# Kernel optimization log

Measured on AMD Instinct MI355X. Metric: run time of the kernel, lower is better.

## Reference

```python
import math
import jax, jax.numpy as jnp
import numpy as np

B, T = 65536, 34
VOCAB, TOK_DIM, POS_DIM, D_MODEL, FFN_DIM, HEAD_DIM = 14, 2, 3, 5, 2, 5
EPS = 1e-5

def _pos_flat_idx():
    # replicate _build_pos_map: 10 digits, Z_HI, 10 digits, Z_HI, 10 digits, special0, special1
    sources, indices = [], []
    for _ in range(3):
        for i in range(10):
            sources.append(0); indices.append(i)
        sources.append(2); indices.append(len([s for s in sources if s == 2]) - 1)
    # fix: the torch code appends (2,0),(2,1) after first two digit blocks and (1,0),(2,2) after the third
    sources, indices = [], []
    for i in range(10): sources.append(0); indices.append(i)
    sources.append(2); indices.append(0)
    for i in range(10): sources.append(0); indices.append(i)
    sources.append(2); indices.append(1)
    for i in range(10): sources.append(0); indices.append(i)
    sources.append(1); indices.append(0)
    sources.append(2); indices.append(2)
    src = np.array(sources); idx = np.array(indices)
    # table layout: rows 0..9 digit_pos, row 10 z_hi_pos, rows 11..13 special (learned0, learned1, eos)
    offs = np.array([0, 10, 11])
    return offs[src] + idx  # (34,)

POS_FLAT = jnp.asarray(_pos_flat_idx())
CAUSAL = jnp.tril(jnp.ones((T, T), dtype=bool))

def _rms(x, w):
    return x * jax.lax.rsqrt(jnp.mean(x * x, -1, keepdims=True) + EPS) * w

def setup_inputs():
    key = jax.random.key(0)
    ks = jax.random.split(key, 16)
    n = lambda i, shape: jax.random.normal(ks[i], shape, jnp.float32) * 0.5
    return {
        'idx': jax.random.randint(ks[0], (B, T), 0, VOCAB),
        'tok_emb': n(1, (VOCAB, TOK_DIM)),
        'spiral_amp': jnp.float32(1.0),
        'spiral_phase': jnp.float32(0.1),
        'spiral_slope': jnp.float32(1.0 / 9.0),
        'spiral_offset': jnp.float32(0.05),
        'pos_corr_slope': jnp.float32(0.01),
        'pos_corr_intercept': jnp.float32(0.02),
        'z_hi_pos': n(2, (1, POS_DIM)),
        'special_pos': n(3, (2, POS_DIM)),
        'q_w': n(4, (HEAD_DIM, POS_DIM)),
        'v_w': n(5, (HEAD_DIM, TOK_DIM)),
        'out_A': n(6, (HEAD_DIM, 2)),
        'out_B': n(7, (2, D_MODEL)),
        'q_phase': n(8, (1,)),
        'ln1_w': jnp.ones((D_MODEL,), jnp.float32),
        'ln2_w': jnp.ones((D_MODEL,), jnp.float32),
        'lnf_w': jnp.ones((D_MODEL,), jnp.float32),
        'fc1_w': n(9, (FFN_DIM, D_MODEL)),
        'fc1_b': n(10, (FFN_DIM,)),
        'fc2_w': n(11, (D_MODEL, FFN_DIM)),
        'fc2_b': n(12, (D_MODEL,)),
        'head_w': n(13, (TOK_DIM, D_MODEL)),
    }

def reference(idx, tok_emb, spiral_amp, spiral_phase, spiral_slope, spiral_offset,
              pos_corr_slope, pos_corr_intercept, z_hi_pos, special_pos,
              q_w, v_w, out_A, out_B, q_phase, ln1_w, ln2_w, lnf_w,
              fc1_w, fc1_b, fc2_w, fc2_b, head_w):
    # learned spiral digit positions (10, 3)
    i = jnp.arange(10, dtype=jnp.float32)
    angle = 2.0 * math.pi * i / 10.0 + spiral_phase
    base = jnp.stack([spiral_amp * jnp.cos(angle),
                      spiral_amp * jnp.sin(angle),
                      spiral_slope * i + spiral_offset], -1)
    corr = pos_corr_intercept + pos_corr_slope * i
    digit_pos = base * (1.0 + corr)[:, None]
    table = jnp.concatenate([digit_pos, z_hi_pos, special_pos,
                             jnp.zeros((1, POS_DIM), jnp.float32)], 0)  # (14, 3)
    pos = table[POS_FLAT]  # (T, 3)

    tok = tok_emb[idx]  # (B, T, 2)
    x = jnp.concatenate([tok, jnp.broadcast_to(pos, (idx.shape[0], T, POS_DIM))], -1)  # (B,T,5)

    h = _rms(x, ln1_w)
    q = jnp.einsum('btp,dp->btd', h[..., TOK_DIM:], q_w)  # (B,T,5)
    k = q  # q_proj applied to same input for both q and k
    v = jnp.einsum('btp,dp->btd', h[..., :TOK_DIM], v_w)  # (B,T,5)

    # per-head 2D rotation on first 4 dims (HEAD_DIM//2 = 2 pairs), dim 4 unchanged
    c, s = jnp.cos(q_phase[0]), jnp.sin(q_phase[0])
    q0, q1 = q[..., 0:4:2], q[..., 1:4:2]
    q_rot = jnp.concatenate([
        jnp.stack([q0 * c - q1 * s, q0 * s + q1 * c], -1).reshape(q.shape[:-1] + (4,)),
        q[..., 4:]], -1)

    att = jnp.einsum('btd,bsd->bts', q_rot, k) / math.sqrt(HEAD_DIM)
    att = jnp.where(CAUSAL, att, -jnp.inf)
    att = jax.nn.softmax(att, -1)
    out = jnp.einsum('bts,bsd->btd', att, v)  # (B,T,5)

    x = x + (out @ out_A) @ out_B  # low-rank out_proj
    hh = _rms(x, ln2_w)
    x = x + (jax.nn.gelu(hh @ fc1_w.T + fc1_b, approximate=False) @ fc2_w.T + fc2_b)
    x = _rms(x, lnf_w)
    return (x @ head_w.T) @ tok_emb.T  # (B, T, 14)
```

## Files before the change

kernel.cpp:

```cpp
#include <hip/hip_runtime.h>
#include <math.h>

#define T_SEQ 34
#define NTOK 14
#define NE (T_SEQ * NTOK)
#define ROWS 32
#define BLK 512
#define RP1 (ROWS + 1)

__global__ __launch_bounds__(BLK) void micro_fused_kernel(
    const int* __restrict__ idx,
    const float* __restrict__ tok_emb,
    const float* __restrict__ s_amp, const float* __restrict__ s_phase,
    const float* __restrict__ s_slope, const float* __restrict__ s_offset,
    const float* __restrict__ pc_slope, const float* __restrict__ pc_int,
    const float* __restrict__ z_hi, const float* __restrict__ spec,
    const float* __restrict__ q_w, const float* __restrict__ v_w,
    const float* __restrict__ out_A, const float* __restrict__ out_B,
    const float* __restrict__ q_phase,
    const float* __restrict__ ln1_w, const float* __restrict__ ln2_w,
    const float* __restrict__ lnf_w,
    const float* __restrict__ fc1_w, const float* __restrict__ fc1_b,
    const float* __restrict__ fc2_w, const float* __restrict__ fc2_b,
    const float* __restrict__ head_w,
    float* __restrict__ out, int N)
{
    __shared__ float4 H4[NE];
    __shared__ float  H1f[NE];
    __shared__ float4 C3[NE];
    __shared__ float4 Gm[T_SEQ * ROWS];
    __shared__ float  G1[T_SEQ * ROWS];
    __shared__ float2 Av[T_SEQ * RP1];
    __shared__ int    toks[ROWS * T_SEQ];
    __shared__ float PosT[T_SEQ * 3];
    __shared__ float TE[NTOK * 2];
    __shared__ float PMs[10];
    __shared__ float Ws[5 * NTOK];
    __shared__ float ln2s[5], lnfs[5], fc1ws[10], fc1bs[2], fc2ws[10], fc2bs[5];

    const int tid = threadIdx.x;
    const int b0 = blockIdx.x * ROWS;
    const int elemBase = b0 * T_SEQ;

    for (int i = tid; i < ROWS * T_SEQ; i += BLK) {
        int g = elemBase + i;
        toks[i] = (g < N) ? idx[g] : 0;
    }

    if (tid < NE) {
        const float amp = s_amp[0], ph = s_phase[0], slp = s_slope[0], off = s_offset[0];
        const float pcs = pc_slope[0], pci = pc_int[0];
        const float cph = cosf(q_phase[0]), sph = sinf(q_phase[0]);
        const float cscale = 0.44721359549995793f * 1.4426950408889634f;
        const int e = tid;
        const int t = e / NTOK, tk = e - t * NTOK;
        float px, py, pz;
        if (t == 33)      { px = 0.f;     py = 0.f;     pz = 0.f; }
        else if (t == 32) { px = z_hi[0]; py = z_hi[1]; pz = z_hi[2]; }
        else if (t == 10) { px = spec[0]; py = spec[1]; pz = spec[2]; }
        else if (t == 21) { px = spec[3]; py = spec[4]; pz = spec[5]; }
        else {
            int i = (t < 10) ? t : (t < 21 ? t - 11 : t - 22);
            float fi = (float)i;
            float ang = 0.62831853071795864769f * fi + ph;
            float mlt = 1.f + pci + pcs * fi;
            px = amp * cosf(ang) * mlt;
            py = amp * sinf(ang) * mlt;
            pz = (slp * fi + off) * mlt;
        }
        if (tk == 0) { PosT[t*3] = px; PosT[t*3+1] = py; PosT[t*3+2] = pz; }
        float x0 = tok_emb[tk * 2], x1 = tok_emb[tk * 2 + 1];
        float ssum = x0*x0 + x1*x1 + px*px + py*py + pz*pz;
        float rn = rsqrtf(ssum * 0.2f + 1e-5f);
        float h0 = x0 * rn * ln1_w[0], h1 = x1 * rn * ln1_w[1];
        float h2 = px * rn * ln1_w[2], h3 = py * rn * ln1_w[3], h4 = pz * rn * ln1_w[4];
        float q0 = q_w[0]  * h2 + q_w[1]  * h3 + q_w[2]  * h4;
        float q1 = q_w[3]  * h2 + q_w[4]  * h3 + q_w[5]  * h4;
        float q2 = q_w[6]  * h2 + q_w[7]  * h3 + q_w[8]  * h4;
        float q3 = q_w[9]  * h2 + q_w[10] * h3 + q_w[11] * h4;
        float q4 = q_w[12] * h2 + q_w[13] * h3 + q_w[14] * h4;
        float r0 = q0 * cph - q1 * sph, r1 = q0 * sph + q1 * cph;
        float r2c = q2 * cph - q3 * sph, r3 = q2 * sph + q3 * cph;
        float c0 = (r0*q_w[0] + r1*q_w[3] + r2c*q_w[6] + r3*q_w[9]  + q4*q_w[12]) * cscale;
        float c1 = (r0*q_w[1] + r1*q_w[4] + r2c*q_w[7] + r3*q_w[10] + q4*q_w[13]) * cscale;
        float c2 = (r0*q_w[2] + r1*q_w[5] + r2c*q_w[8] + r3*q_w[11] + q4*q_w[14]) * cscale;
        H4[e] = make_float4(h2, h3, h4, h0);
        H1f[e] = h1;
        C3[e] = make_float4(c0, c1, c2, 0.f);
    }
    if (tid < 28) TE[tid] = tok_emb[tid];
    if (tid < 70) {
        int d = tid / NTOK, v = tid - d * NTOK;
        Ws[tid] = head_w[d] * tok_emb[v * 2] + head_w[5 + d] * tok_emb[v * 2 + 1];
    }
    if (tid < 10) {
        int j = tid >> 1, c = tid & 1;
        float acc = 0.f;
        for (int i = 0; i < 5; ++i) {
            float m5 = out_A[i*2] * out_B[j] + out_A[i*2+1] * out_B[5 + j];
            acc += m5 * v_w[i*2 + c];
        }
        PMs[tid] = acc;
    }
    if (tid < 5)  { ln2s[tid] = ln2_w[tid]; lnfs[tid] = lnf_w[tid]; fc2bs[tid] = fc2_b[tid]; }
    if (tid < 10) { fc1ws[tid] = fc1_w[tid]; fc2ws[tid] = fc2_w[tid]; }
    if (tid < 2)  { fc1bs[tid] = fc1_b[tid]; }

    __syncthreads();

    for (int i = tid; i < T_SEQ * ROWS; i += BLK) {
        int s = i >> 5;
        int r = i & (ROWS - 1);
        int tok = toks[r * T_SEQ + s];
        int e = s * NTOK + tok;
        Gm[i] = H4[e];
        G1[i] = H1f[e];
    }
    __syncthreads();

    for (int ii = tid; ii < T_SEQ * ROWS; ii += BLK) {
        int t = ii >> 5;
        int r = ii & (ROWS - 1);
        int tok = toks[r * T_SEQ + t];
        float4 c3 = C3[t * NTOK + tok];
        float l = 0.f, a0 = 0.f, a1 = 0.f;
        const float4* gm = &Gm[r];
        const float*  g1 = &G1[r];
#pragma unroll 4
        for (int s = 0; s <= t; ++s) {
            float4 h  = gm[s * ROWS];
            float h1v = g1[s * ROWS];
            float sc = fmaf(c3.x, h.x, fmaf(c3.y, h.y, c3.z * h.z));
            float p = exp2f(sc);
            l += p;
            a0 = fmaf(p, h.w, a0);
            a1 = fmaf(p, h1v, a1);
        }
        float il = 1.f / l;
        Av[t * RP1 + r] = make_float2(a0 * il, a1 * il);
    }
    __syncthreads();

    for (int e2 = tid; e2 < ROWS * T_SEQ; e2 += BLK) {
        int lin = elemBase + e2;
        if (lin >= N) break;
        int r = e2 / T_SEQ;
        int t = e2 - r * T_SEQ;
        int tok = toks[e2];
        float2 a = Av[t * RP1 + r];
        float xv0 = TE[tok * 2], xv1 = TE[tok * 2 + 1];
        float xv2 = PosT[t*3], xv3 = PosT[t*3+1], xv4 = PosT[t*3+2];

        float y[5];
#pragma unroll
        for (int j = 0; j < 5; ++j)
            y[j] = (j == 0 ? xv0 : j == 1 ? xv1 : j == 2 ? xv2 : j == 3 ? xv3 : xv4)
                 + PMs[j*2] * a.x + PMs[j*2+1] * a.y;

        float s2 = y[0]*y[0] + y[1]*y[1] + y[2]*y[2] + y[3]*y[3] + y[4]*y[4];
        float r2 = rsqrtf(s2 * 0.2f + 1e-5f);
        float hh[5];
#pragma unroll
        for (int j = 0; j < 5; ++j) hh[j] = y[j] * r2 * ln2s[j];

        float u0 = fc1bs[0], u1 = fc1bs[1];
#pragma unroll
        for (int j = 0; j < 5; ++j) { u0 += hh[j] * fc1ws[j]; u1 += hh[j] * fc1ws[5 + j]; }
        float g0 = 0.5f * u0 * (1.f + erff(u0 * 0.70710678118654752f));
        float g1v = 0.5f * u1 * (1.f + erff(u1 * 0.70710678118654752f));

        float y2[5]; float s3 = 0.f;
#pragma unroll
        for (int j = 0; j < 5; ++j) {
            y2[j] = y[j] + g0 * fc2ws[j * 2] + g1v * fc2ws[j * 2 + 1] + fc2bs[j];
            s3 += y2[j] * y2[j];
        }
        float r3 = rsqrtf(s3 * 0.2f + 1e-5f);
        float z[5];
#pragma unroll
        for (int j = 0; j < 5; ++j) z[j] = y2[j] * r3 * lnfs[j];

        float res[14];
#pragma unroll
        for (int v = 0; v < 14; ++v)
            res[v] = z[0] * Ws[v] + z[1] * Ws[14 + v] + z[2] * Ws[28 + v]
                   + z[3] * Ws[42 + v] + z[4] * Ws[56 + v];

        float2* op = (float2*)(out + (size_t)lin * 14);
#pragma unroll
        for (int v = 0; v < 7; ++v) op[v] = make_float2(res[2 * v], res[2 * v + 1]);
    }
}

extern "C" void kernel_launch(void* const* d_in, const int* in_sizes, int n_in,
                              void* d_out, int out_size, void* d_ws, size_t ws_size,
                              hipStream_t stream) {
    const int N = in_sizes[0];
    const int grid = (N + ROWS * T_SEQ - 1) / (ROWS * T_SEQ);
    micro_fused_kernel<<<grid, BLK, 0, stream>>>(
        (const int*)d_in[0],
        (const float*)d_in[1], (const float*)d_in[2], (const float*)d_in[3],
        (const float*)d_in[4], (const float*)d_in[5], (const float*)d_in[6],
        (const float*)d_in[7], (const float*)d_in[8], (const float*)d_in[9],
        (const float*)d_in[10], (const float*)d_in[11], (const float*)d_in[12],
        (const float*)d_in[13], (const float*)d_in[14], (const float*)d_in[15],
        (const float*)d_in[16], (const float*)d_in[17], (const float*)d_in[18],
        (const float*)d_in[19], (const float*)d_in[20], (const float*)d_in[21],
        (const float*)d_in[22],
        (float*)d_out, N);
}
```

Before: 248.2 us.

## Drop gathered key staging and pair causal rows for balanced attention work

Removes the Gm/G1 staging pass and its barrier. The attention loop now gathers H4/H1f directly through a transposed, padded token table. Work is assigned by pairing query position t with 33-t, so each thread gets a similar causal loop length, and positions 16/17 go to the first 64 threads. Launch bounds request higher occupancy and shared memory shrinks, at the cost of an extra indirect LDS lookup per inner iteration, which may cause bank conflicts on the random H4 gathers.

Measured after the change: 427.8 us. 72.4% more time.

```diff
diff --git a/kernel.cpp b/kernel.cpp
--- a/kernel.cpp
+++ b/kernel.cpp
@@ -6,9 +6,10 @@
 #define NE (T_SEQ * NTOK)
 #define ROWS 32
 #define BLK 512
-#define RP1 (ROWS + 1)
-
-__global__ __launch_bounds__(BLK) void micro_fused_kernel(
+#define AVS (ROWS + 1)
+#define TTS (ROWS + 1)
+
+__global__ __launch_bounds__(BLK, 8) void micro_fused_kernel(
     const int* __restrict__ idx,
     const float* __restrict__ tok_emb,
     const float* __restrict__ s_amp, const float* __restrict__ s_phase,
@@ -28,10 +29,8 @@
     __shared__ float4 H4[NE];
     __shared__ float  H1f[NE];
     __shared__ float4 C3[NE];
-    __shared__ float4 Gm[T_SEQ * ROWS];
-    __shared__ float  G1[T_SEQ * ROWS];
-    __shared__ float2 Av[T_SEQ * RP1];
-    __shared__ int    toks[ROWS * T_SEQ];
+    __shared__ float2 Av[T_SEQ * AVS];
+    __shared__ int    toksT[T_SEQ * TTS];
     __shared__ float PosT[T_SEQ * 3];
     __shared__ float TE[NTOK * 2];
     __shared__ float PMs[10];
@@ -44,7 +43,9 @@
 
     for (int i = tid; i < ROWS * T_SEQ; i += BLK) {
         int g = elemBase + i;
-        toks[i] = (g < N) ? idx[g] : 0;
+        int v = (g < N) ? idx[g] : 0;
+        int r = i / T_SEQ, s = i - r * T_SEQ;
+        toksT[s * TTS + r] = v;
     }
 
     if (tid < NE) {
@@ -108,28 +109,16 @@
 
     __syncthreads();
 
-    for (int i = tid; i < T_SEQ * ROWS; i += BLK) {
-        int s = i >> 5;
-        int r = i & (ROWS - 1);
-        int tok = toks[r * T_SEQ + s];
-        int e = s * NTOK + tok;
-        Gm[i] = H4[e];
-        G1[i] = H1f[e];
-    }
-    __syncthreads();
-
-    for (int ii = tid; ii < T_SEQ * ROWS; ii += BLK) {
-        int t = ii >> 5;
-        int r = ii & (ROWS - 1);
-        int tok = toks[r * T_SEQ + t];
-        float4 c3 = C3[t * NTOK + tok];
+    auto attn = [&](int t, int rr) {
+        int tokt = toksT[t * TTS + rr];
+        float4 c3 = C3[t * NTOK + tokt];
         float l = 0.f, a0 = 0.f, a1 = 0.f;
-        const float4* gm = &Gm[r];
-        const float*  g1 = &G1[r];
-#pragma unroll 4
+#pragma unroll 2
         for (int s = 0; s <= t; ++s) {
-            float4 h  = gm[s * ROWS];
-            float h1v = g1[s * ROWS];
+            int tok = toksT[s * TTS + rr];
+            int e = s * NTOK + tok;
+            float4 h = H4[e];
+            float h1v = H1f[e];
             float sc = fmaf(c3.x, h.x, fmaf(c3.y, h.y, c3.z * h.z));
             float p = exp2f(sc);
             l += p;
@@ -137,17 +126,25 @@
             a1 = fmaf(p, h1v, a1);
         }
         float il = 1.f / l;
-        Av[t * RP1 + r] = make_float2(a0 * il, a1 * il);
-    }
+        Av[t * AVS + rr] = make_float2(a0 * il, a1 * il);
+    };
+
+    const int r = tid & 31;
+    const int tg = tid >> 5;
+    attn(tg, r);
+    attn(33 - tg, r);
+    if (tid < 64)
+        attn(16 + (tid >> 5), tid & 31);
+
     __syncthreads();
 
     for (int e2 = tid; e2 < ROWS * T_SEQ; e2 += BLK) {
         int lin = elemBase + e2;
         if (lin >= N) break;
-        int r = e2 / T_SEQ;
-        int t = e2 - r * T_SEQ;
-        int tok = toks[e2];
-        float2 a = Av[t * RP1 + r];
+        int rr = e2 / T_SEQ;
+        int t = e2 - rr * T_SEQ;
+        int tok = toksT[t * TTS + rr];
+        float2 a = Av[t * AVS + rr];
         float xv0 = TE[tok * 2], xv1 = TE[tok * 2 + 1];
         float xv2 = PosT[t*3], xv3 = PosT[t*3+1], xv4 = PosT[t*3+2];
 
```
